# Performance work log

Measured on AMD Instinct MI355X. Metric: run time of the kernel, lower is better.

## Reference

```python
import jax, jax.numpy as jnp
import numpy as np

NSTEP = 5

# Clauses (vals = one-hot satisfying truth value per literal):
#   clause 0: ~S(x) | C(x)          vals: L0=[1,0], L1=[0,1]
#   clause 1: ~F(x,y) | ~S(x) | S(y) vals: L0=[1,0], L1=[1,0], L2=[0,1]
# Message to target literal i (torch influence()):
#   msg = w[r] * einsum over shared vars of prod_j ( q[pn_j] . (1 - vals_j) ) outer t_vals

def setup_inputs() -> dict:
    B, N = 2, 2048
    key = jax.random.key(0)
    k1, k2, k3 = jax.random.split(key, 3)
    return {
        "logits_S": jax.random.normal(k1, (B, N, 2), jnp.float32),
        "logits_C": jax.random.normal(k2, (B, N, 2), jnp.float32),
        "logits_F": jax.random.normal(k3, (B, N, N, 2), jnp.float32),
        "weights": jnp.ones((2,), jnp.float32),
    }


def _messages(qS, qC, qF, weights):
    dt = qS.dtype
    e_true = jnp.array([0.0, 1.0], dtype=dt)   # one-hot: positive literal satisfied
    e_false = jnp.array([1.0, 0.0], dtype=dt)  # one-hot: negated literal satisfied
    w0, w1 = weights[0], weights[1]
    # clause 0: ~S(x) | C(x)
    msg_C = (w0 * qS[..., 1])[..., None] * e_true            # [B,N,2]
    msg_S = (w0 * qC[..., 0])[..., None] * e_false           # [B,N,2]
    # clause 1: ~F(x,y) | ~S(x) | S(y)
    # target F(x,y): (q_S[b,x,true]) * (q_S[b,y,false]) on the 'false' slot of F
    msg_F = (w1 * qS[:, :, None, 1] * qS[:, None, :, 0])[..., None] * e_false  # [B,N,N,2]
    # target ~S(x): sum_y q_F[b,x,y,true] * q_S[b,y,false]
    msg_S = msg_S + (w1 * jnp.einsum('bxy,by->bx', qF[..., 1], qS[..., 0]))[..., None] * e_false
    # target S(y): sum_x q_F[b,x,y,true] * q_S[b,x,true]
    msg_S = msg_S + (w1 * jnp.einsum('bxy,bx->by', qF[..., 1], qS[..., 1]))[..., None] * e_true
    return msg_S, msg_C, msg_F


def reference(logits_S, logits_C, logits_F, weights):
    cur_S, cur_C, cur_F = logits_S, logits_C, logits_F
    for _ in range(NSTEP):
        qS = jax.nn.softmax(cur_S, axis=-1)
        qC = jax.nn.softmax(cur_C, axis=-1)
        qF = jax.nn.softmax(cur_F, axis=-1)
        msg_S, msg_C, msg_F = _messages(qS, qC, qF, weights)
        cur_S = logits_S + msg_S
        cur_C = logits_C + msg_C
        cur_F = logits_F + msg_F
    return (cur_S, cur_C, cur_F)
```

## Files before the change

### kernel.cpp

```cpp
#include <hip/hip_runtime.h>

#define BB 2
#define NN 2048
#define ROWS (BB*NN)
#define RPB 16
#define CSPLIT 4
#define NCSL 8
#define NRSL 2

__device__ __forceinline__ float fsig(float x) {
    float e = __expf(-x);
    return __builtin_amdgcn_rcpf(1.0f + e);
}

__global__ void ksmall(const float* __restrict__ S, const float* __restrict__ C,
                       const float* __restrict__ w,
                       float* __restrict__ rpart, float* __restrict__ cpart,
                       const float* __restrict__ aS_prev, float* __restrict__ aS_cur,
                       float* __restrict__ qC0, int first)
{
    int idx = blockIdx.x * blockDim.x + threadIdx.x;
    if (idx >= ROWS) return;
    float w0 = w[0], w1 = w[1];
    float2 sv = ((const float2*)S)[idx];
    float2 cv = ((const float2*)C)[idx];
    float aS, qc;
    if (first) {
        aS = fsig(sv.y - sv.x);
        qc = fsig(cv.x - cv.y);
#pragma unroll
        for (int s = 0; s < NRSL; s++) rpart[s*ROWS + idx] = 0.0f;
#pragma unroll
        for (int s = 0; s < NCSL; s++) cpart[s*ROWS + idx] = 0.0f;
    } else {
        float rs = 0.0f;
#pragma unroll
        for (int s = 0; s < NRSL; s++) { rs += rpart[s*ROWS + idx]; rpart[s*ROWS + idx] = 0.0f; }
        float cs = 0.0f;
#pragma unroll
        for (int s = 0; s < NCSL; s++) { cs += cpart[s*ROWS + idx]; cpart[s*ROWS + idx] = 0.0f; }
        float ap  = aS_prev[idx];
        float qcp = qC0[idx];
        float s0 = sv.x + w0*qcp + w1*rs;
        float s1 = sv.y + w1*cs;
        aS = fsig(s1 - s0);
        qc = fsig(cv.x - cv.y - w0*ap);
    }
    aS_cur[idx] = aS;
    qC0[idx]    = qc;
}

template<int MODE>
__global__ __launch_bounds__(256) void kbig(
    const float4* __restrict__ F,
    const float* __restrict__ aS_cur, const float* __restrict__ aS_prev,
    const float* __restrict__ w,
    float* __restrict__ rpart, float* __restrict__ cpart,
    float4* __restrict__ outF)
{
    const int tid  = threadIdx.x;
    const int sx   = blockIdx.x;
    const int by   = blockIdx.y;
    const int j    = sx * 256 + tid;
    const int row0 = by * RPB;
    const int b    = row0 >> 11;
    const int lane = tid & 63;
    const float w1 = w[1];

    float* rdst = rpart + (sx & (NRSL-1)) * ROWS;
    float* cdst = cpart + (by & (NCSL-1)) * ROWS;

    const float wq0 = 1.0f - aS_cur[b*NN + 2*j];
    const float wq1 = 1.0f - aS_cur[b*NN + 2*j + 1];
    float bp0 = 0.0f, bp1 = 0.0f;
    if (MODE != 0) {
        bp0 = 1.0f - aS_prev[b*NN + 2*j];
        bp1 = 1.0f - aS_prev[b*NN + 2*j + 1];
    }

    float c0 = 0.0f, c1 = 0.0f;

#pragma unroll 4
    for (int i = 0; i < RPB; i++) {
        const int row = row0 + i;
        const int x   = row & (NN - 1);
        const float a_c = aS_cur[b*NN + x];
        float m1 = 0.0f;
        if (MODE != 0) m1 = w1 * aS_prev[b*NN + x];

        const float4 f = F[(size_t)row * (NN/2) + j];
        const float d0 = f.y - f.x;
        const float d1 = f.w - f.z;
        float s0, s1;
        if (MODE == 0) { s0 = fsig(d0); s1 = fsig(d1); }
        else           { s0 = fsig(d0 - m1*bp0); s1 = fsig(d1 - m1*bp1); }

        c0 += s0 * a_c;
        c1 += s1 * a_c;

        if (MODE == 2) {
            const float mw = w1 * a_c;
            float4 o;
            o.x = f.x + mw*wq0;
            o.y = f.y;
            o.z = f.z + mw*wq1;
            o.w = f.w;
            outF[(size_t)row * (NN/2) + j] = o;
        }

        float ra = s0*wq0 + s1*wq1;
#pragma unroll
        for (int off = 32; off > 0; off >>= 1) ra += __shfl_down(ra, off);
        if (lane == 0) atomicAdd(&rdst[row], ra);
    }

    atomicAdd(&cdst[b*NN + 2*j],     c0);
    atomicAdd(&cdst[b*NN + 2*j + 1], c1);
}

__global__ void kfin(const float* __restrict__ S, const float* __restrict__ C,
                     const float* __restrict__ w,
                     const float* __restrict__ rpart, const float* __restrict__ cpart,
                     const float* __restrict__ aS4, const float* __restrict__ qC0,
                     float* __restrict__ outS, float* __restrict__ outC)
{
    int idx = blockIdx.x * blockDim.x + threadIdx.x;
    if (idx >= ROWS) return;
    float w0 = w[0], w1 = w[1];
    float rs = 0.0f;
#pragma unroll
    for (int s = 0; s < NRSL; s++) rs += rpart[s*ROWS + idx];
    float cs = 0.0f;
#pragma unroll
    for (int s = 0; s < NCSL; s++) cs += cpart[s*ROWS + idx];
    float2 sv = ((const float2*)S)[idx];
    float2 cv = ((const float2*)C)[idx];
    float2 os, oc;
    os.x = sv.x + w0*qC0[idx] + w1*rs;
    os.y = sv.y + w1*cs;
    oc.x = cv.x;
    oc.y = cv.y + w0*aS4[idx];
    ((float2*)outS)[idx] = os;
    ((float2*)outC)[idx] = oc;
}

extern "C" void kernel_launch(void* const* d_in, const int* in_sizes, int n_in,
                              void* d_out, int out_size, void* d_ws, size_t ws_size,
                              hipStream_t stream)
{
    const float* S = (const float*)d_in[0];
    const float* C = (const float*)d_in[1];
    const float* F = (const float*)d_in[2];
    const float* w = (const float*)d_in[3];
    float* out = (float*)d_out;
    float* ws  = (float*)d_ws;

    float* rpart = ws;
    float* cpart = ws + NRSL*ROWS;
    float* aSA   = ws + (NRSL+NCSL)*ROWS;
    float* aSB   = aSA + ROWS;
    float* qC0   = aSB + ROWS;

    const float4* F4 = (const float4*)F;
    float* outS = out;
    float* outC = out + 2*ROWS;
    float4* outF = (float4*)(out + 4*ROWS);

    dim3 gs(ROWS/256), bs(256);
    dim3 gb(CSPLIT, ROWS/RPB), bbk(256);

    ksmall<<<gs, bs, 0, stream>>>(S, C, w, rpart, cpart, aSB, aSA, qC0, 1);
    kbig<0><<<gb, bbk, 0, stream>>>(F4, aSA, aSB, w, rpart, cpart, nullptr);
    ksmall<<<gs, bs, 0, stream>>>(S, C, w, rpart, cpart, aSA, aSB, qC0, 0);
    kbig<1><<<gb, bbk, 0, stream>>>(F4, aSB, aSA, w, rpart, cpart, nullptr);
    ksmall<<<gs, bs, 0, stream>>>(S, C, w, rpart, cpart, aSB, aSA, qC0, 0);
    kbig<1><<<gb, bbk, 0, stream>>>(F4, aSA, aSB, w, rpart, cpart, nullptr);
    ksmall<<<gs, bs, 0, stream>>>(S, C, w, rpart, cpart, aSA, aSB, qC0, 0);
    kbig<1><<<gb, bbk, 0, stream>>>(F4, aSB, aSA, w, rpart, cpart, nullptr);
    ksmall<<<gs, bs, 0, stream>>>(S, C, w, rpart, cpart, aSB, aSA, qC0, 0);
    kbig<2><<<gb, bbk, 0, stream>>>(F4, aSA, aSB, w, rpart, cpart, outF);
    kfin<<<gs, bs, 0, stream>>>(S, C, w, rpart, cpart, aSA, qC0, outS, outC);
}
```

Before: 207.0 us.

## Fuse per-step small kernel into big F kernel with LDS row reductions

Removes the separate ksmall launches by having each kbig block recompute the S/C state it needs from the previous step's partial sums, using per-step buffers so no clearing race occurs. The next step's column buffer is zeroed inside the kernel. Row sums now go through an LDS tile with plain stores per column split instead of shuffle plus atomics. This cuts launches and atomics, but each block redundantly recomputes sigmoids for 528 entries and reads more partial buffers.

```diff
diff --git a/kernel.cpp b/kernel.cpp
--- a/kernel.cpp
+++ b/kernel.cpp
@@ -1,183 +1,177 @@
 #include <hip/hip_runtime.h>
 
-#define BB 2
-#define NN 2048
-#define ROWS (BB*NN)
-#define RPB 16
+#define NN   2048
+#define ROWS 4096
+#define RPB  16
 #define CSPLIT 4
+#define NBY  (ROWS/RPB)
 #define NCSL 8
-#define NRSL 2
+#define PSTR 257
 
 __device__ __forceinline__ float fsig(float x) {
     float e = __expf(-x);
     return __builtin_amdgcn_rcpf(1.0f + e);
 }
 
-__global__ void ksmall(const float* __restrict__ S, const float* __restrict__ C,
-                       const float* __restrict__ w,
-                       float* __restrict__ rpart, float* __restrict__ cpart,
-                       const float* __restrict__ aS_prev, float* __restrict__ aS_cur,
-                       float* __restrict__ qC0, int first)
-{
-    int idx = blockIdx.x * blockDim.x + threadIdx.x;
-    if (idx >= ROWS) return;
-    float w0 = w[0], w1 = w[1];
-    float2 sv = ((const float2*)S)[idx];
-    float2 cv = ((const float2*)C)[idx];
-    float aS, qc;
-    if (first) {
-        aS = fsig(sv.y - sv.x);
-        qc = fsig(cv.x - cv.y);
-#pragma unroll
-        for (int s = 0; s < NRSL; s++) rpart[s*ROWS + idx] = 0.0f;
-#pragma unroll
-        for (int s = 0; s < NCSL; s++) cpart[s*ROWS + idx] = 0.0f;
-    } else {
-        float rs = 0.0f;
-#pragma unroll
-        for (int s = 0; s < NRSL; s++) { rs += rpart[s*ROWS + idx]; rpart[s*ROWS + idx] = 0.0f; }
-        float cs = 0.0f;
-#pragma unroll
-        for (int s = 0; s < NCSL; s++) { cs += cpart[s*ROWS + idx]; cpart[s*ROWS + idx] = 0.0f; }
-        float ap  = aS_prev[idx];
-        float qcp = qC0[idx];
-        float s0 = sv.x + w0*qcp + w1*rs;
-        float s1 = sv.y + w1*cs;
-        aS = fsig(s1 - s0);
-        qc = fsig(cv.x - cv.y - w0*ap);
-    }
-    aS_cur[idx] = aS;
-    qC0[idx]    = qc;
-}
-
-template<int MODE>
+template<int T>
 __global__ __launch_bounds__(256) void kbig(
     const float4* __restrict__ F,
-    const float* __restrict__ aS_cur, const float* __restrict__ aS_prev,
+    const float2* __restrict__ S2, const float2* __restrict__ C2,
     const float* __restrict__ w,
-    float* __restrict__ rpart, float* __restrict__ cpart,
+    const float* __restrict__ rprev, const float* __restrict__ cprev,
+    const float* __restrict__ aSm1, const float* __restrict__ aSm2,
+    float* __restrict__ rout, float* __restrict__ cout,
+    float* __restrict__ czero, float* __restrict__ aSout,
     float4* __restrict__ outF)
 {
+    __shared__ float sCur[528];
+    __shared__ float sPrev[528];
+    __shared__ float part[16 * PSTR];
+
     const int tid  = threadIdx.x;
     const int sx   = blockIdx.x;
     const int by   = blockIdx.y;
-    const int j    = sx * 256 + tid;
     const int row0 = by * RPB;
-    const int b    = row0 >> 11;
-    const int lane = tid & 63;
-    const float w1 = w[1];
+    const int b    = by >> 7;
+    const int bloc = by & 127;
+    const int base = b * NN;
+    const float w0 = w[0], w1 = w[1];
 
-    float* rdst = rpart + (sx & (NRSL-1)) * ROWS;
-    float* cdst = cpart + (by & (NCSL-1)) * ROWS;
+    if (T < 4 && sx == 1) {
+        int zi = by * 256 + tid;
+        if (zi < NCSL * ROWS) czero[zi] = 0.0f;
+    }
 
-    const float wq0 = 1.0f - aS_cur[b*NN + 2*j];
-    const float wq1 = 1.0f - aS_cur[b*NN + 2*j + 1];
-    float bp0 = 0.0f, bp1 = 0.0f;
-    if (MODE != 0) {
-        bp0 = 1.0f - aS_prev[b*NN + 2*j];
-        bp1 = 1.0f - aS_prev[b*NN + 2*j + 1];
+    for (int idx = tid; idx < 528; idx += 256) {
+        int il = (idx < 512) ? (sx * 512 + idx) : (bloc * RPB + idx - 512);
+        int g  = base + il;
+        float2 sv = S2[g];
+        float a0 = fsig(sv.y - sv.x);
+        float cur, prev;
+        if (T == 0) {
+            cur = a0; prev = 0.0f;
+        } else {
+            float2 cv = C2[g];
+            float rs = rprev[0*ROWS+g] + rprev[1*ROWS+g]
+                     + rprev[2*ROWS+g] + rprev[3*ROWS+g];
+            float cs = 0.0f;
+#pragma unroll
+            for (int s = 0; s < NCSL; s++) cs += cprev[s*ROWS + g];
+            float qc;
+            if (T == 1)      qc = fsig(cv.x - cv.y);
+            else if (T == 2) qc = fsig(cv.x - cv.y - w0 * a0);
+            else             qc = fsig(cv.x - cv.y - w0 * aSm2[g]);
+            cur  = fsig((sv.y + w1*cs) - (sv.x + w0*qc + w1*rs));
+            prev = (T == 1) ? a0 : aSm1[g];
+        }
+        sCur[idx]  = cur;
+        sPrev[idx] = prev;
+        if (T >= 1 && sx == 0 && idx >= 512) aSout[g] = cur;
     }
+    __syncthreads();
+
+    const int j = sx * 256 + tid;
+    const float wq0 = 1.0f - sCur[2*tid];
+    const float wq1 = 1.0f - sCur[2*tid + 1];
+    const float bp0 = 1.0f - sPrev[2*tid];
+    const float bp1 = 1.0f - sPrev[2*tid + 1];
 
     float c0 = 0.0f, c1 = 0.0f;
 
 #pragma unroll 4
     for (int i = 0; i < RPB; i++) {
-        const int row = row0 + i;
-        const int x   = row & (NN - 1);
-        const float a_c = aS_cur[b*NN + x];
-        float m1 = 0.0f;
-        if (MODE != 0) m1 = w1 * aS_prev[b*NN + x];
-
-        const float4 f = F[(size_t)row * (NN/2) + j];
-        const float d0 = f.y - f.x;
-        const float d1 = f.w - f.z;
-        float s0, s1;
-        if (MODE == 0) { s0 = fsig(d0); s1 = fsig(d1); }
-        else           { s0 = fsig(d0 - m1*bp0); s1 = fsig(d1 - m1*bp1); }
-
+        const float a_c = sCur[512 + i];
+        const float m1  = (T == 0) ? 0.0f : w1 * sPrev[512 + i];
+        const float4 f = F[(size_t)(row0 + i) * (NN/2) + j];
+        float s0 = fsig((f.y - f.x) - m1 * bp0);
+        float s1 = fsig((f.w - f.z) - m1 * bp1);
         c0 += s0 * a_c;
         c1 += s1 * a_c;
-
-        if (MODE == 2) {
+        part[i * PSTR + tid] = s0 * wq0 + s1 * wq1;
+        if (T == 4) {
             const float mw = w1 * a_c;
             float4 o;
-            o.x = f.x + mw*wq0;
-            o.y = f.y;
-            o.z = f.z + mw*wq1;
-            o.w = f.w;
-            outF[(size_t)row * (NN/2) + j] = o;
+            o.x = f.x + mw * wq0; o.y = f.y;
+            o.z = f.z + mw * wq1; o.w = f.w;
+            outF[(size_t)(row0 + i) * (NN/2) + j] = o;
         }
-
-        float ra = s0*wq0 + s1*wq1;
-#pragma unroll
-        for (int off = 32; off > 0; off >>= 1) ra += __shfl_down(ra, off);
-        if (lane == 0) atomicAdd(&rdst[row], ra);
     }
 
-    atomicAdd(&cdst[b*NN + 2*j],     c0);
-    atomicAdd(&cdst[b*NN + 2*j + 1], c1);
+    atomicAdd(&cout[(by & (NCSL-1))*ROWS + base + 2*j],     c0);
+    atomicAdd(&cout[(by & (NCSL-1))*ROWS + base + 2*j + 1], c1);
+
+    __syncthreads();
+    {
+        const int row = tid >> 4, seg = tid & 15;
+        float s = 0.0f;
+#pragma unroll
+        for (int u = 0; u < 16; u++) s += part[row * PSTR + seg * 16 + u];
+#pragma unroll
+        for (int off = 8; off > 0; off >>= 1) s += __shfl_down(s, off, 16);
+        if (seg == 0) rout[sx * ROWS + row0 + row] = s;
+    }
 }
 
-__global__ void kfin(const float* __restrict__ S, const float* __restrict__ C,
+__global__ void kfin(const float2* __restrict__ S2, const float2* __restrict__ C2,
                      const float* __restrict__ w,
                      const float* __restrict__ rpart, const float* __restrict__ cpart,
-                     const float* __restrict__ aS4, const float* __restrict__ qC0,
-                     float* __restrict__ outS, float* __restrict__ outC)
+                     const float* __restrict__ aS4, const float* __restrict__ aS3,
+                     float2* __restrict__ outS, float2* __restrict__ outC)
 {
     int idx = blockIdx.x * blockDim.x + threadIdx.x;
     if (idx >= ROWS) return;
     float w0 = w[0], w1 = w[1];
-    float rs = 0.0f;
-#pragma unroll
-    for (int s = 0; s < NRSL; s++) rs += rpart[s*ROWS + idx];
+    float rs = rpart[0*ROWS+idx] + rpart[1*ROWS+idx]
+             + rpart[2*ROWS+idx] + rpart[3*ROWS+idx];
     float cs = 0.0f;
 #pragma unroll
     for (int s = 0; s < NCSL; s++) cs += cpart[s*ROWS + idx];
-    float2 sv = ((const float2*)S)[idx];
-    float2 cv = ((const float2*)C)[idx];
+    float2 sv = S2[idx], cv = C2[idx];
+    float qc4 = fsig(cv.x - cv.y - w0 * aS3[idx]);
     float2 os, oc;
-    os.x = sv.x + w0*qC0[idx] + w1*rs;
-    os.y = sv.y + w1*cs;
+    os.x = sv.x + w0 * qc4 + w1 * rs;
+    os.y = sv.y + w1 * cs;
     oc.x = cv.x;
-    oc.y = cv.y + w0*aS4[idx];
-    ((float2*)outS)[idx] = os;
-    ((float2*)outC)[idx] = oc;
+    oc.y = cv.y + w0 * aS4[idx];
+    outS[idx] = os;
+    outC[idx] = oc;
 }
 
 extern "C" void kernel_launch(void* const* d_in, const int* in_sizes, int n_in,
                               void* d_out, int out_size, void* d_ws, size_t ws_size,
                               hipStream_t stream)
 {
-    const float* S = (const float*)d_in[0];
-    const float* C = (const float*)d_in[1];
-    const float* F = (const float*)d_in[2];
-    const float* w = (const float*)d_in[3];
+    const float2* S2 = (const float2*)d_in[0];
+    const float2* C2 = (const float2*)d_in[1];
+    const float4* F4 = (const float4*)d_in[2];
+    const float*  w  = (const float*)d_in[3];
     float* out = (float*)d_out;
     float* ws  = (float*)d_ws;
 
-    float* rpart = ws;
-    float* cpart = ws + NRSL*ROWS;
-    float* aSA   = ws + (NRSL+NCSL)*ROWS;
-    float* aSB   = aSA + ROWS;
-    float* qC0   = aSB + ROWS;
+    float* rb = ws;
+    float* cb = ws + 5 * 4 * ROWS;
+    float* ab = ws + 5 * 4 * ROWS + 5 * 8 * ROWS;
+#define RB(t) (rb + (t) * 4 * ROWS)
+#define CB(t) (cb + (t) * (size_t)NCSL * ROWS)
+#define AB(t) (ab + ((t) - 1) * ROWS)
 
-    const float4* F4 = (const float4*)F;
     float* outS = out;
-    float* outC = out + 2*ROWS;
-    float4* outF = (float4*)(out + 4*ROWS);
+    float* outC = out + 2 * ROWS;
+    float4* outF = (float4*)(out + 4 * ROWS);
 
-    dim3 gs(ROWS/256), bs(256);
-    dim3 gb(CSPLIT, ROWS/RPB), bbk(256);
+    hipMemsetAsync(CB(0), 0, (size_t)NCSL * ROWS * sizeof(float), stream);
 
-    ksmall<<<gs, bs, 0, stream>>>(S, C, w, rpart, cpart, aSB, aSA, qC0, 1);
-    kbig<0><<<gb, bbk, 0, stream>>>(F4, aSA, aSB, w, rpart, cpart, nullptr);
-    ksmall<<<gs, bs, 0, stream>>>(S, C, w, rpart, cpart, aSA, aSB, qC0, 0);
-    kbig<1><<<gb, bbk, 0, stream>>>(F4, aSB, aSA, w, rpart, cpart, nullptr);
-    ksmall<<<gs, bs, 0, stream>>>(S, C, w, rpart, cpart, aSB, aSA, qC0, 0);
-    kbig<1><<<gb, bbk, 0, stream>>>(F4, aSA, aSB, w, rpart, cpart, nullptr);
-    ksmall<<<gs, bs, 0, stream>>>(S, C, w, rpart, cpart, aSA, aSB, qC0, 0);
-    kbig<1><<<gb, bbk, 0, stream>>>(F4, aSB, aSA, w, rpart, cpart, nullptr);
-    ksmall<<<gs, bs, 0, stream>>>(S, C, w, rpart, cpart, aSB, aSA, qC0, 0);
-    kbig<2><<<gb, bbk, 0, stream>>>(F4, aSA, aSB, w, rpart, cpart, outF);
-    kfin<<<gs, bs, 0, stream>>>(S, C, w, rpart, cpart, aSA, qC0, outS, outC);
+    dim3 gb(CSPLIT, NBY), bb(256);
+    kbig<0><<<gb, bb, 0, stream>>>(F4, S2, C2, w, nullptr, nullptr, nullptr, nullptr,
+                                   RB(0), CB(0), CB(1), nullptr, nullptr);
+    kbig<1><<<gb, bb, 0, stream>>>(F4, S2, C2, w, RB(0), CB(0), nullptr, nullptr,
+                                   RB(1), CB(1), CB(2), AB(1), nullptr);
+    kbig<2><<<gb, bb, 0, stream>>>(F4, S2, C2, w, RB(1), CB(1), AB(1), nullptr,
+                                   RB(2), CB(2), CB(3), AB(2), nullptr);
+    kbig<3><<<gb, bb, 0, stream>>>(F4, S2, C2, w, RB(2), CB(2), AB(2), AB(1),
+                                   RB(3), CB(3), CB(4), AB(3), nullptr);
+    kbig<4><<<gb, bb, 0, stream>>>(F4, S2, C2, w, RB(3), CB(3), AB(3), AB(2),
+                                   RB(4), CB(4), nullptr, AB(4), outF);
+    kfin<<<dim3(ROWS/256), bb, 0, stream>>>(S2, C2, w, RB(4), CB(4), AB(4), AB(3),
+                                            (float2*)outS, (float2*)outC);
 }
```

Result: faster. 186.5 us (-9.9%).
